# Optimization experiments

Measured on AMD Instinct MI355X. Metric: run time of the kernel, lower is better.

Reference implementation:

```python
import jax, jax.numpy as jnp
import numpy as np
from jax import lax

HEADS = 8
DIM_HEAD = 64
INNER = HEADS * DIM_HEAD  # 512
DIM = 256
TOP_K = 512  # top_k=-1 -> Lk // heads = 4096 // 8
LN_EPS = 1e-5


def chan_ln(x, g, b):
    # LayerNorm over channel dim (axis=1) of [b,c,D,H,W]
    mu = jnp.mean(x, axis=1, keepdims=True)
    var = jnp.mean((x - mu) ** 2, axis=1, keepdims=True)
    xn = (x - mu) * lax.rsqrt(var + LN_EPS)
    return xn * g[None, :, None, None, None] + b[None, :, None, None, None]


def l1_cdist(K, Q):
    # K: [B,N,D], Q: [B,M,D] -> [B,N,M]; scan over feature dim to avoid a [B,N,M,D] intermediate
    Kt = jnp.moveaxis(K, -1, 0)  # [D,B,N]
    Qt = jnp.moveaxis(Q, -1, 0)  # [D,B,M]
    acc0 = jnp.zeros((K.shape[0], K.shape[1], Q.shape[1]), K.dtype)
    def step(acc, kq):
        kd, qd = kq
        return acc + jnp.abs(kd[:, :, None] - qd[:, None, :]), None
    acc, _ = lax.scan(step, acc0, (Kt, Qt))
    return acc


def l2norm_ax(t, axis):
    n = jnp.sqrt(jnp.sum(t * t, axis=axis, keepdims=True))
    return t / jnp.maximum(n, 1e-12)


def setup_inputs() -> dict:
    key = jax.random.key(0)
    ks = jax.random.split(key, 12)
    b, Dq, Hq, Wq = 2, 16, 32, 32
    Dc, Hc, Wc = 16, 16, 16
    Lk = Dc * Hc * Wc  # 4096
    return {
        "query_source": jax.random.normal(ks[0], (b, DIM, Dq, Hq, Wq), jnp.float32),
        "context": jax.random.normal(ks[1], (b, DIM, Dc, Hc, Wc), jnp.float32),
        "rand_idx": jax.random.randint(ks[2], (b * HEADS, TOP_K), 0, 4096),
        "g_ctx": jnp.ones((DIM,), jnp.float32),
        "b_ctx": jnp.zeros((DIM,), jnp.float32),
        "g_qs": jnp.ones((DIM,), jnp.float32),
        "b_qs": jnp.zeros((DIM,), jnp.float32),
        "w_kv": jax.random.normal(ks[3], (2 * INNER, DIM), jnp.float32) * 0.02,
        "w_q": jax.random.normal(ks[4], (INNER, DIM), jnp.float32) * 0.02,
        "w_out": jax.random.normal(ks[5], (DIM, INNER), jnp.float32) * 0.02,
        "g_out": jnp.ones((DIM,), jnp.float32),
        "b_out": jnp.zeros((DIM,), jnp.float32),
        "gamma": jnp.full((1,), 0.5, jnp.float32),
    }


def reference(query_source, context, rand_idx, g_ctx, b_ctx, g_qs, b_qs,
              w_kv, w_q, w_out, g_out, b_out, gamma):
    b, c, Dq, Hq, Wq = query_source.shape
    Lq = Dq * Hq * Wq
    Lk = context.shape[2] * context.shape[3] * context.shape[4]

    ctx = chan_ln(context, g_ctx, b_ctx)
    qsn = chan_ln(query_source, g_qs, b_qs)

    # 1x1x1 convs == channel matmuls
    kv = jnp.einsum('oc,bcdhw->bodhw', w_kv, ctx)
    k, v = jnp.split(kv, 2, axis=1)
    q = jnp.einsum('oc,bcdhw->bodhw', w_q, qsn)

    def fold(t):  # [b, inner, ...] -> [b, heads, dim_head, L]
        return t.reshape(t.shape[0], HEADS, DIM_HEAD, -1)
    q, k, v = fold(q), fold(k), fold(v)
    # l2norm over dim_head channels (torch dim=1 after (b h) fold)
    q = l2norm_ax(q, 2)
    k = l2norm_ax(k, 2)
    # -> [b, heads, L, dim_head]
    q = jnp.swapaxes(q, 2, 3)
    k = jnp.swapaxes(k, 2, 3)
    v = jnp.swapaxes(v, 2, 3)

    BH = b * HEADS
    qf = q.reshape(BH, Lq, DIM_HEAD)
    kf = k.reshape(BH, Lk, DIM_HEAD)
    vf = v.reshape(BH, Lk, DIM_HEAD)

    # random-query-anchored token pruning
    Q_small = jnp.take_along_axis(qf, rand_idx[:, :, None], axis=1)  # [BH, TOP_K, dh]
    dist = l1_cdist(kf, Q_small)                                     # [BH, Lk, TOP_K]
    min_d = jnp.min(dist, axis=2)                                    # [BH, Lk]
    _, idx = lax.top_k(-min_d, TOP_K)                                # smallest distances
    ks_sel = jnp.take_along_axis(kf, idx[:, :, None], axis=1)        # [BH, TOP_K, dh]
    vs_sel = jnp.take_along_axis(vf, idx[:, :, None], axis=1)

    ks4 = ks_sel.reshape(b, HEADS, TOP_K, DIM_HEAD)
    vs4 = vs_sel.reshape(b, HEADS, TOP_K, DIM_HEAD)

    # SDPA with scale=1.0, no dropout (eval)
    scores = jnp.einsum('bhqd,bhkd->bhqk', q, ks4)
    attn = jax.nn.softmax(scores, axis=-1)
    out = jnp.einsum('bhqk,bhkd->bhqd', attn, vs4)  # [b,H,Lq,dh]

    out = out.reshape(b, HEADS, Dq, Hq, Wq, DIM_HEAD)
    out = jnp.transpose(out, (0, 1, 5, 2, 3, 4)).reshape(b, INNER, Dq, Hq, Wq)
    out = jnp.einsum('oc,bcdhw->bodhw', w_out, out)
    out = chan_ln(out, g_out, b_out)
    return gamma[0] * out + query_source
```

## Files before the change

kernel.cpp:

```cpp
#include <hip/hip_runtime.h>
#include <hip/hip_bf16.h>
#include <math.h>

#define DIMC  256
#define HEADS 8
#define DH    64
#define INNER 512
#define TOPK  512
#define LQ    16384
#define LKE   4096
#define NB    2
#define NBH   16

typedef __attribute__((ext_vector_type(8))) short bf16x8;
typedef __attribute__((ext_vector_type(4))) float f32x4;
typedef __attribute__((ext_vector_type(16))) unsigned u32x16;

__device__ __forceinline__ unsigned short f2bf(float f) {
    unsigned u = __float_as_uint(f);
    u += 0x7FFFu + ((u >> 16) & 1u);
    return (unsigned short)(u >> 16);
}
__device__ __forceinline__ float bf2f(unsigned short b) {
    return __uint_as_float(((unsigned)b) << 16);
}
__device__ __forceinline__ f32x4 mfma16(bf16x8 a, bf16x8 b, f32x4 c) {
    return __builtin_amdgcn_mfma_f32_16x16x32_bf16(a, b, c, 0, 0, 0);
}
__device__ __forceinline__ unsigned f2q16(float v) {
    return (unsigned)((int)rintf(v * 32000.0f) + 32768) & 0xFFFFu;
}

__global__ void stats_kernel(const float* __restrict__ x, float* __restrict__ mu,
                             float* __restrict__ rs, int L, int total) {
    int idx = blockIdx.x * 256 + threadIdx.x;
    if (idx >= total) return;
    int b = idx / L, l = idx - b * L;
    const float* p = x + (size_t)b * DIMC * L + l;
    float s = 0.f, sq = 0.f;
    for (int c = 0; c < DIMC; c++) {
        float v = p[(size_t)c * L];
        s += v; sq += v * v;
    }
    float m = s * (1.0f / DIMC);
    float var = fmaxf(sq * (1.0f / DIMC) - m * m, 0.f);
    mu[idx] = m;
    rs[idx] = rsqrtf(var + 1e-5f);
}

template<bool WRITELO>
__global__ __launch_bounds__(256) void ln_transpose_kernel(
    const float* __restrict__ x, const float* __restrict__ mu, const float* __restrict__ rs,
    const float* __restrict__ g, const float* __restrict__ beta, int L,
    unsigned short* __restrict__ xhi, unsigned short* __restrict__ xlo) {
    int lt = blockIdx.x, ct = blockIdx.y, b = blockIdx.z;
    int l0 = lt * 64, c0 = ct * 64;
    int t = threadIdx.x;
    __shared__ float T[64][65];
#pragma unroll
    for (int r = 0; r < 16; r++) {
        int f = r * 256 + t;
        int l = f & 63, c = f >> 6;
        int loc = b * L + l0 + l;
        float v = x[((size_t)b * DIMC + c0 + c) * L + l0 + l];
        T[c][l] = (v - mu[loc]) * rs[loc] * g[c0 + c] + beta[c0 + c];
    }
    __syncthreads();
#pragma unroll
    for (int r = 0; r < 16; r++) {
        int f = r * 256 + t;
        int c = f & 63, l = f >> 6;
        float v = T[c][l];
        unsigned short hi = f2bf(v);
        size_t di = ((size_t)b * L + l0 + l) * DIMC + c0 + c;
        xhi[di] = hi;
        if (WRITELO) xlo[di] = f2bf(v - bf2f(hi));
    }
}

template<int MODE>
__global__ __launch_bounds__(256) void gemm_mfma_kernel(
    const float* __restrict__ wmat,
    const unsigned short* __restrict__ xhi, const unsigned short* __restrict__ xlo,
    void* __restrict__ dst0, void* __restrict__ dst1, void* __restrict__ dst2) {
    constexpr int K = (MODE == 2) ? 512 : 256;
    constexpr int N = (MODE == 0) ? LKE : LQ;
    constexpr bool MAYSPLIT = (MODE == 0);
    int n0 = blockIdx.x * 128;
    int by = blockIdx.y;
    int bb = blockIdx.z;
    int t = threadIdx.x, w = t >> 6, lane = t & 63;
    int wm = w >> 1, wn = w & 1;
    int lanelo = lane & 15, lanehi = lane >> 4;

    __shared__ __align__(16) char Wh[16384];
    __shared__ __align__(16) char Xh[16384];
    __shared__ __align__(16) char Wl[MAYSPLIT ? 16384 : 16];
    __shared__ __align__(16) char Xl[MAYSPLIT ? 16384 : 16];

    bool split = MAYSPLIT && (by < 4);

    const float* wsrc = wmat + (size_t)by * 128 * K;
    const unsigned short* xsh = xhi + ((size_t)bb * N + n0) * K;
    const unsigned short* xsl = xlo + ((size_t)bb * N + n0) * K;

    f32x4 acc[4][4];
#pragma unroll
    for (int mi = 0; mi < 4; mi++)
#pragma unroll
        for (int ni = 0; ni < 4; ni++) acc[mi][ni] = (f32x4){0.f, 0.f, 0.f, 0.f};

    for (int k0 = 0; k0 < K; k0 += 64) {
        if (k0) __syncthreads();
#pragma unroll
        for (int gg = 0; gg < 4; gg++) {
            int e = gg * 2048 + t * 8;
            int row = e >> 6, kc = e & 63;
            const float* wp = wsrc + (size_t)row * K + k0 + kc;
            bf16x8 hi, lo;
#pragma unroll
            for (int i = 0; i < 8; i++) {
                float v = wp[i];
                unsigned short h = f2bf(v);
                hi[i] = (short)h;
                if (MAYSPLIT) lo[i] = (short)f2bf(v - bf2f(h));
            }
            int off = (row * 128 + kc * 2) ^ ((row & 7) << 4);
            *(bf16x8*)(Wh + off) = hi;
            *(bf16x8*)(Xh + off) = *(const bf16x8*)(xsh + (size_t)row * K + k0 + kc);
            if (split) {
                *(bf16x8*)(Wl + off) = lo;
                *(bf16x8*)(Xl + off) = *(const bf16x8*)(xsl + (size_t)row * K + k0 + kc);
            }
        }
        __syncthreads();
#pragma unroll
        for (int kk = 0; kk < 2; kk++) {
            bf16x8 ah[4], bh_[4];
#pragma unroll
            for (int mi = 0; mi < 4; mi++) {
                int row = wm * 64 + mi * 16 + lanelo;
                int off = (row * 128 + kk * 64 + lanehi * 16) ^ ((row & 7) << 4);
                ah[mi] = *(const bf16x8*)(Wh + off);
            }
#pragma unroll
            for (int ni = 0; ni < 4; ni++) {
                int row = wn * 64 + ni * 16 + lanelo;
                int off = (row * 128 + kk * 64 + lanehi * 16) ^ ((row & 7) << 4);
                bh_[ni] = *(const bf16x8*)(Xh + off);
            }
#pragma unroll
            for (int mi = 0; mi < 4; mi++)
#pragma unroll
                for (int ni = 0; ni < 4; ni++)
                    acc[mi][ni] = mfma16(ah[mi], bh_[ni], acc[mi][ni]);
            if (split) {
                bf16x8 al[4], bl_[4];
#pragma unroll
                for (int mi = 0; mi < 4; mi++) {
                    int row = wm * 64 + mi * 16 + lanelo;
                    int off = (row * 128 + kk * 64 + lanehi * 16) ^ ((row & 7) << 4);
                    al[mi] = *(const bf16x8*)(Wl + off);
                }
#pragma unroll
                for (int ni = 0; ni < 4; ni++) {
                    int row = wn * 64 + ni * 16 + lanelo;
                    int off = (row * 128 + kk * 64 + lanehi * 16) ^ ((row & 7) << 4);
                    bl_[ni] = *(const bf16x8*)(Xl + off);
                }
#pragma unroll
                for (int mi = 0; mi < 4; mi++)
#pragma unroll
                    for (int ni = 0; ni < 4; ni++) {
                        acc[mi][ni] = mfma16(ah[mi], bl_[ni], acc[mi][ni]);
                        acc[mi][ni] = mfma16(al[mi], bh_[ni], acc[mi][ni]);
                    }
            }
        }
    }

    bool donorm = (MODE == 1) || (MODE == 0 && by < 4);
    float inv[4];
    if (donorm) {
#pragma unroll
        for (int ni = 0; ni < 4; ni++) {
            float s = 0.f;
#pragma unroll
            for (int mi = 0; mi < 4; mi++)
#pragma unroll
                for (int rg = 0; rg < 4; rg++) s += acc[mi][ni][rg] * acc[mi][ni][rg];
            s += __shfl_xor(s, 16);
            s += __shfl_xor(s, 32);
            inv[ni] = 1.0f / fmaxf(sqrtf(s), 1e-12f);
        }
    }
#pragma unroll
    for (int mi = 0; mi < 4; mi++) {
        int rowg = by * 128 + wm * 64 + mi * 16 + lanehi * 4;
#pragma unroll
        for (int ni = 0; ni < 4; ni++) {
            int l = n0 + wn * 64 + ni * 16 + lanelo;
            if (MODE == 0) {
                bool isk = rowg < 512;
                float sc = isk ? inv[ni] : 1.0f;
                int h = (rowg >> 6) & 7, d0 = rowg & 63;
                float4 v = make_float4(acc[mi][ni][0] * sc, acc[mi][ni][1] * sc,
                                       acc[mi][ni][2] * sc, acc[mi][ni][3] * sc);
                float* dp = isk ? (float*)dst0 : (float*)dst1;
                size_t base = ((size_t)(bb * HEADS + h) * LKE + l) * 64 + d0;
                *(float4*)&dp[base] = v;
                if (isk) {
                    uint2 pk;
                    pk.x = f2q16(v.x) | (f2q16(v.y) << 16);
                    pk.y = f2q16(v.z) | (f2q16(v.w) << 16);
                    *(uint2*)&((unsigned*)dst2)[(((size_t)(bb * HEADS + h) * LKE + l) * 64 + d0) / 2] = pk;
                }
            } else if (MODE == 1) {
                int h = rowg >> 6, d0 = rowg & 63;
                ushort4 u;
                u.x = f2bf(acc[mi][ni][0] * inv[ni]);
                u.y = f2bf(acc[mi][ni][1] * inv[ni]);
                u.z = f2bf(acc[mi][ni][2] * inv[ni]);
                u.w = f2bf(acc[mi][ni][3] * inv[ni]);
                unsigned short* qp = (unsigned short*)dst0;
                *(ushort4*)&qp[((size_t)(bb * HEADS + h) * LQ + l) * 64 + d0] = u;
            } else {
                float4 v = make_float4(acc[mi][ni][0], acc[mi][ni][1],
                                       acc[mi][ni][2], acc[mi][ni][3]);
                float* pp = (float*)dst0;
                *(float4*)&pp[((size_t)bb * LQ + l) * 256 + rowg] = v;
            }
        }
    }
}

__global__ __launch_bounds__(256) void qsample_kernel(
    const float* __restrict__ x, const float* __restrict__ mu, const float* __restrict__ rs,
    const float* __restrict__ g, const float* __restrict__ beta,
    const float* __restrict__ w, const int* __restrict__ ridx,
    unsigned* __restrict__ Qint) {
    int lt = blockIdx.x, bh = blockIdx.y;
    int b = bh >> 3, h = bh & 7;
    int t = threadIdx.x, tx = t & 15, ty = t >> 4;
    __shared__ float Ws[64][33];
    __shared__ float Xs[32][65];
    __shared__ float Cs[64][65];
    __shared__ float nf[64];
    __shared__ int lidx[64];
    if (t < 64) lidx[t] = ridx[bh * TOPK + lt * 64 + t];
    __syncthreads();
    float acc[4][4];
#pragma unroll
    for (int a = 0; a < 4; a++)
#pragma unroll
        for (int c2 = 0; c2 < 4; c2++) acc[a][c2] = 0.f;
    for (int kc = 0; kc < DIMC; kc += 32) {
#pragma unroll
        for (int r = 0; r < 8; r++) {
            int f = r * 256 + t;
            int oi = f >> 5, kj = f & 31;
            Ws[oi][kj] = w[(size_t)(h * 64 + oi) * DIMC + kc + kj];
        }
#pragma unroll
        for (int r = 0; r < 8; r++) {
            int f = r * 256 + t;
            int kj = f >> 6, lj = f & 63;
            int l = lidx[lj];
            int loc = b * LQ + l;
            float v = x[(size_t)b * DIMC * LQ + (size_t)(kc + kj) * LQ + l];
            Xs[kj][lj] = (v - mu[loc]) * rs[loc] * g[kc + kj] + beta[kc + kj];
        }
        __syncthreads();
#pragma unroll
        for (int kj = 0; kj < 32; kj++) {
            float wr[4], xr[4];
#pragma unroll
            for (int a = 0; a < 4; a++) wr[a] = Ws[ty * 4 + a][kj];
#pragma unroll
            for (int c2 = 0; c2 < 4; c2++) xr[c2] = Xs[kj][tx * 4 + c2];
#pragma unroll
            for (int a = 0; a < 4; a++)
#pragma unroll
                for (int c2 = 0; c2 < 4; c2++) acc[a][c2] += wr[a] * xr[c2];
        }
        __syncthreads();
    }
#pragma unroll
    for (int a = 0; a < 4; a++)
#pragma unroll
        for (int c2 = 0; c2 < 4; c2++) Cs[ty * 4 + a][tx * 4 + c2] = acc[a][c2];
    __syncthreads();
    if (t < 64) {
        float sq = 0.f;
        for (int o = 0; o < 64; o++) { float v = Cs[o][t]; sq += v * v; }
        nf[t] = 1.0f / fmaxf(sqrtf(sq), 1e-12f);
    }
    __syncthreads();
#pragma unroll
    for (int r = 0; r < 8; r++) {
        int f = r * 256 + t;
        int dp = f & 31, lj = f >> 5;
        float v0 = Cs[dp * 2][lj] * nf[lj];
        float v1 = Cs[dp * 2 + 1][lj] * nf[lj];
        Qint[((size_t)bh * TOPK + (size_t)lt * 64 + lj) * 32 + dp] =
            f2q16(v0) | (f2q16(v1) << 16);
    }
}

__global__ __launch_bounds__(256) __attribute__((amdgpu_waves_per_eu(4, 4)))
void cdist_sad_kernel(
    const unsigned* __restrict__ kint,
    const unsigned* __restrict__ Qint,
    unsigned* __restrict__ min_d4) {
    int bh = blockIdx.y;
    int key = blockIdx.x * 256 + threadIdx.x;
    int qz = blockIdx.z;
    const unsigned* kp = kint + ((size_t)bh * LKE + key) * 32;
    unsigned k[32];
#pragma unroll
    for (int d8 = 0; d8 < 8; d8++) {
        uint4 v = *(const uint4*)(kp + d8 * 4);
        k[d8 * 4 + 0] = v.x; k[d8 * 4 + 1] = v.y;
        k[d8 * 4 + 2] = v.z; k[d8 * 4 + 3] = v.w;
    }
#pragma unroll
    for (int d = 0; d < 32; d++) asm volatile("" : "+v"(k[d]));

    unsigned long long qaddr = (unsigned long long)(const void*)
        (Qint + ((size_t)bh * TOPK + (size_t)qz * (TOPK / 4)) * 32);
    u32x16 qa0, qa1, qb0, qb1;
    asm volatile(
        "s_load_dwordx16 %0, %2, 0x00\n\t"
        "s_load_dwordx16 %1, %2, 0x40"
        : "=s"(qa0), "=s"(qa1) : "s"(qaddr));
    unsigned best = 0xFFFFFFFFu;

#define S1(ACC, KK, QQ) asm("v_sad_u16 %0, %1, %2, %0" : "+v"(ACC) : "v"(KK), "s"(QQ));
#define S16(QV, KB) \
    S1(a0, k[KB + 0], QV[0])  S1(a1, k[KB + 1], QV[1]) \
    S1(a2, k[KB + 2], QV[2])  S1(a3, k[KB + 3], QV[3]) \
    S1(a0, k[KB + 4], QV[4])  S1(a1, k[KB + 5], QV[5]) \
    S1(a2, k[KB + 6], QV[6])  S1(a3, k[KB + 7], QV[7]) \
    S1(a0, k[KB + 8], QV[8])  S1(a1, k[KB + 9], QV[9]) \
    S1(a2, k[KB + 10], QV[10]) S1(a3, k[KB + 11], QV[11]) \
    S1(a0, k[KB + 12], QV[12]) S1(a1, k[KB + 13], QV[13]) \
    S1(a2, k[KB + 14], QV[14]) S1(a3, k[KB + 15], QV[15])

    for (int qi = 0; qi < TOPK / 4; qi += 2) {
        asm volatile(
            "s_load_dwordx16 %0, %2, 0x80\n\t"
            "s_load_dwordx16 %1, %2, 0xc0"
            : "=s"(qb0), "=s"(qb1) : "s"(qaddr));
        asm volatile("s_waitcnt lgkmcnt(2)" : "+s"(qa0), "+s"(qa1));
        {
            unsigned a0 = 0, a1 = 0, a2 = 0, a3 = 0;
            S16(qa0, 0) S16(qa1, 16)
            best = min(best, (a0 + a1) + (a2 + a3));
        }
        qaddr += 256;
        asm volatile(
            "s_load_dwordx16 %0, %2, 0x00\n\t"
            "s_load_dwordx16 %1, %2, 0x40"
            : "=s"(qa0), "=s"(qa1) : "s"(qaddr));
        asm volatile("s_waitcnt lgkmcnt(2)" : "+s"(qb0), "+s"(qb1));
        {
            unsigned a0 = 0, a1 = 0, a2 = 0, a3 = 0;
            S16(qb0, 0) S16(qb1, 16)
            best = min(best, (a0 + a1) + (a2 + a3));
        }
    }
#undef S16
#undef S1
    min_d4[((size_t)qz * NBH + bh) * LKE + key] = best;
}

__global__ void select_topk_kernel(const unsigned* __restrict__ min_d4, int* __restrict__ isel) {
    int bh = blockIdx.x;
    int t = threadIdx.x;
    __shared__ unsigned su[LKE];
    __shared__ int hist[256];
    __shared__ int sb[2];
    for (int i = t; i < LKE; i += 256) {
        unsigned a = min(min_d4[(size_t)bh * LKE + i],
                         min_d4[(size_t)(NBH + bh) * LKE + i]);
        unsigned b = min(min_d4[(size_t)(2 * NBH + bh) * LKE + i],
                         min_d4[(size_t)(3 * NBH + bh) * LKE + i]);
        su[i] = min(a, b);
    }
    unsigned prefix = 0, mask = 0;
    int need = TOPK;
    for (int shift = 24; shift >= 0; shift -= 8) {
        hist[t] = 0;
        __syncthreads();
        for (int i = t; i < LKE; i += 256) {
            unsigned u = su[i];
            if ((u & mask) == prefix) atomicAdd(&hist[(u >> shift) & 255], 1);
        }
        __syncthreads();
        if (t == 0) {
            int c = 0, bsel = 0;
            for (; bsel < 255; bsel++) {
                if (c + hist[bsel] >= need) break;
                c += hist[bsel];
            }
            sb[0] = bsel; sb[1] = need - c;
        }
        __syncthreads();
        prefix |= ((unsigned)sb[0]) << shift;
        mask |= (255u << shift);
        need = sb[1];
        __syncthreads();
    }
    if (t < 64) {
        int pos = 0, eqseen = 0;
        unsigned long long lanem1 = (t == 0) ? 0ull : ((1ull << t) - 1ull);
        for (int i0 = 0; i0 < LKE; i0 += 64) {
            unsigned u = su[i0 + t];
            bool lt = (u < prefix);
            bool eq = (u == prefix);
            unsigned long long be = __ballot(eq);
            int eqbefore = __popcll(be & lanem1);
            bool take = lt || (eq && (eqseen + eqbefore) < need);
            unsigned long long bt = __ballot(take);
            if (take) isel[bh * TOPK + pos + __popcll(bt & lanem1)] = i0 + t;
            pos += __popcll(bt);
            eqseen += __popcll(be);
        }
    }
}

__global__ void gather_k_kernel(const float* __restrict__ kf, const int* __restrict__ isel,
                                unsigned short* __restrict__ kselh) {
    int idx = blockIdx.x * 256 + threadIdx.x;
    int d = idx & 63;
    int ti = (idx >> 6) & (TOPK - 1);
    int bh = idx >> 15;
    int row = isel[bh * TOPK + ti];
    kselh[idx] = f2bf(kf[((size_t)bh * LKE + row) * 64 + d]);
}

__global__ __launch_bounds__(256) void gather_vT_kernel(
    const float* __restrict__ vf, const int* __restrict__ isel,
    unsigned short* __restrict__ vTh) {
    int bh = blockIdx.y, kc = blockIdx.x * 64;
    int t = threadIdx.x;
    __shared__ float T[64][65];
#pragma unroll
    for (int r = 0; r < 4; r++) {
        int c = r * 256 + t;
        int row = c >> 4, c4 = c & 15;
        int krow = isel[bh * TOPK + kc + row];
        float4 v = *(const float4*)(vf + ((size_t)bh * LKE + krow) * 64 + c4 * 4);
        T[row][c4 * 4 + 0] = v.x; T[row][c4 * 4 + 1] = v.y;
        T[row][c4 * 4 + 2] = v.z; T[row][c4 * 4 + 3] = v.w;
    }
    __syncthreads();
#pragma unroll
    for (int r = 0; r < 16; r++) {
        int f = r * 256 + t;
        int d = f >> 6, key = f & 63;
        vTh[(size_t)bh * 64 * TOPK + (size_t)d * TOPK + kc + key] = f2bf(T[key][d]);
    }
}

__global__ __launch_bounds__(256) void attn_mfma_kernel(
    const unsigned short* __restrict__ qh,
    const unsigned short* __restrict__ kselh,
    const unsigned short* __restrict__ vTh,
    unsigned short* __restrict__ afT) {
    int bh = blockIdx.y, rt = blockIdx.x;
    int bq = bh >> 3, h = bh & 7;
    int t = threadIdx.x, w = t >> 6, lane = t & 63;
    __shared__ unsigned short Qs[64 * 64];
    __shared__ unsigned short Ks[2][64 * 64];
    __shared__ unsigned short Vts[2][64 * 64];
    __shared__ unsigned short Ps[4 * 16 * 64];

    const unsigned short* qb = qh + ((size_t)bh * LQ + (size_t)rt * 64) * 64;
    const unsigned short* kb = kselh + (size_t)bh * TOPK * 64;
    const unsigned short* vb = vTh + (size_t)bh * 64 * TOPK;

    int row0s = t >> 3, c80 = t & 7;
    int row1s = 32 + (t >> 3), c81 = t & 7;
    int offs0 = (row0s * 128 + c80 * 16) ^ ((row0s & 7) << 4);
    int offs1 = (row1s * 128 + c81 * 16) ^ ((row1s & 7) << 4);

    {
        bf16x8 v0 = *(const bf16x8*)(qb + row0s * 64 + c80 * 8);
        bf16x8 v1 = *(const bf16x8*)(qb + row1s * 64 + c81 * 8);
        *(bf16x8*)((char*)Qs + offs0) = v0;
        *(bf16x8*)((char*)Qs + offs1) = v1;
    }
    {
        bf16x8 k0 = *(const bf16x8*)(kb + row0s * 64 + c80 * 8);
        bf16x8 k1 = *(const bf16x8*)(kb + row1s * 64 + c81 * 8);
        bf16x8 v0 = *(const bf16x8*)(vb + row0s * TOPK + c80 * 8);
        bf16x8 v1 = *(const bf16x8*)(vb + row1s * TOPK + c81 * 8);
        *(bf16x8*)((char*)Ks[0] + offs0) = k0;
        *(bf16x8*)((char*)Ks[0] + offs1) = k1;
        *(bf16x8*)((char*)Vts[0] + offs0) = v0;
        *(bf16x8*)((char*)Vts[0] + offs1) = v1;
    }
    __syncthreads();

    bf16x8 qfrag[2];
#pragma unroll
    for (int kk = 0; kk < 2; kk++) {
        int row = w * 16 + (lane & 15);
        qfrag[kk] = *(const bf16x8*)((char*)Qs +
            ((row * 128 + kk * 64 + (lane >> 4) * 16) ^ ((row & 7) << 4)));
    }

    f32x4 o[4];
#pragma unroll
    for (int m = 0; m < 4; m++) o[m] = (f32x4){0.f, 0.f, 0.f, 0.f};
    float part[4] = {0.f, 0.f, 0.f, 0.f};
    unsigned short* pw = Ps + w * 16 * 64;
    int cur = 0;

    for (int ch = 0; ch < 8; ch++) {
        bf16x8 knx0, knx1, vnx0, vnx1;
        if (ch < 7) {
            int kc0 = (ch + 1) * 64;
            knx0 = *(const bf16x8*)(kb + (kc0 + row0s) * 64 + c80 * 8);
            knx1 = *(const bf16x8*)(kb + (kc0 + row1s) * 64 + c81 * 8);
            vnx0 = *(const bf16x8*)(vb + row0s * TOPK + kc0 + c80 * 8);
            vnx1 = *(const bf16x8*)(vb + row1s * TOPK + kc0 + c81 * 8);
        }
        f32x4 s[4];
#pragma unroll
        for (int n = 0; n < 4; n++) {
            s[n] = (f32x4){0.f, 0.f, 0.f, 0.f};
#pragma unroll
            for (int kk = 0; kk < 2; kk++) {
                int row = n * 16 + (lane & 15);
                bf16x8 kfr = *(const bf16x8*)((char*)Ks[cur] +
                    ((row * 128 + kk * 64 + (lane >> 4) * 16) ^ ((row & 7) << 4)));
                s[n] = mfma16(qfrag[kk], kfr, s[n]);
            }
        }
#pragma unroll
        for (int n = 0; n < 4; n++) {
#pragma unroll
            for (int rg = 0; rg < 4; rg++) {
                float p = __expf(s[n][rg]);
                part[rg] += p;
                int row = (lane >> 4) * 4 + rg, col = n * 16 + (lane & 15);
                *(unsigned short*)((char*)pw +
                    ((row * 128 + col * 2) ^ ((row & 7) << 4))) = f2bf(p);
            }
        }
        bf16x8 pfrag[2];
#pragma unroll
        for (int kk = 0; kk < 2; kk++) {
            int row = lane & 15;
            pfrag[kk] = *(const bf16x8*)((char*)pw +
                ((row * 128 + kk * 64 + (lane >> 4) * 16) ^ ((row & 7) << 4)));
        }
#pragma unroll
        for (int m = 0; m < 4; m++) {
#pragma unroll
            for (int kk = 0; kk < 2; kk++) {
                int row = m * 16 + (lane & 15);
                bf16x8 vfr = *(const bf16x8*)((char*)Vts[cur] +
                    ((row * 128 + kk * 64 + (lane >> 4) * 16) ^ ((row & 7) << 4)));
                o[m] = mfma16(pfrag[kk], vfr, o[m]);
            }
        }
        if (ch < 7) {
            *(bf16x8*)((char*)Ks[cur ^ 1] + offs0) = knx0;
            *(bf16x8*)((char*)Ks[cur ^ 1] + offs1) = knx1;
            *(bf16x8*)((char*)Vts[cur ^ 1] + offs0) = vnx0;
            *(bf16x8*)((char*)Vts[cur ^ 1] + offs1) = vnx1;
        }
        __syncthreads();
        cur ^= 1;
    }
    float lsum[4];
#pragma unroll
    for (int rg = 0; rg < 4; rg++) {
        float v = part[rg];
        v += __shfl_xor(v, 1); v += __shfl_xor(v, 2);
        v += __shfl_xor(v, 4); v += __shfl_xor(v, 8);
        lsum[rg] = v;
    }
    int row0 = w * 16 + (lane >> 4) * 4;
#pragma unroll
    for (int rg = 0; rg < 4; rg++) {
        float invs = 1.0f / lsum[rg];
        int l = rt * 64 + row0 + rg;
        size_t base = ((size_t)bq * LQ + l) * 512 + h * 64 + (lane & 15);
#pragma unroll
        for (int m = 0; m < 4; m++)
            afT[base + m * 16] = f2bf(o[m][rg] * invs);
    }
}

__global__ void stats_loc_kernel(const float* __restrict__ pre, float* __restrict__ mu,
                                 float* __restrict__ rs) {
    int t = threadIdx.x;
    int grp = t >> 4, ln = t & 15;
    int loc = blockIdx.x * 16 + grp;
    const float4* p = (const float4*)(pre + (size_t)loc * 256);
    float s = 0.f, sq = 0.f;
#pragma unroll
    for (int i = 0; i < 4; i++) {
        float4 v = p[ln + i * 16];
        s += v.x + v.y + v.z + v.w;
        sq += v.x * v.x + v.y * v.y + v.z * v.z + v.w * v.w;
    }
#pragma unroll
    for (int d = 1; d < 16; d <<= 1) {
        s += __shfl_xor(s, d);
        sq += __shfl_xor(sq, d);
    }
    if (ln == 0) {
        float m = s * (1.0f / 256.0f);
        float var = fmaxf(sq * (1.0f / 256.0f) - m * m, 0.f);
        mu[loc] = m;
        rs[loc] = rsqrtf(var + 1e-5f);
    }
}

__global__ __launch_bounds__(256) void final_kernel(
    const float* __restrict__ pre, const float* __restrict__ mu,
    const float* __restrict__ rs, const float* __restrict__ g,
    const float* __restrict__ beta, const float* __restrict__ gamma,
    const float* __restrict__ qs_in, float* __restrict__ out) {
    int lt = blockIdx.x, ot = blockIdx.y, b = blockIdx.z;
    int l0 = lt * 64, o0 = ot * 64;
    int t = threadIdx.x;
    __shared__ float T[64][65];
    float gm = gamma[0];
#pragma unroll
    for (int r = 0; r < 16; r++) {
        int f = r * 256 + t;
        int o = f & 63, l = f >> 6;
        int loc = b * LQ + l0 + l;
        float v = pre[(size_t)loc * 256 + o0 + o];
        T[o][l] = ((v - mu[loc]) * rs[loc] * g[o0 + o] + beta[o0 + o]) * gm;
    }
    __syncthreads();
#pragma unroll
    for (int r = 0; r < 16; r++) {
        int f = r * 256 + t;
        int l = f & 63, o = f >> 6;
        size_t oi = ((size_t)(b * DIMC + o0 + o)) * LQ + l0 + l;
        out[oi] = T[o][l] + qs_in[oi];
    }
}

extern "C" void kernel_launch(void* const* d_in, const int* in_sizes, int n_in,
                              void* d_out, int out_size, void* d_ws, size_t ws_size,
                              hipStream_t stream) {
    const float* qs_in = (const float*)d_in[0];
    const float* ctx   = (const float*)d_in[1];
    const int*   ridx  = (const int*)d_in[2];
    const float* g_ctx = (const float*)d_in[3];
    const float* b_ctx = (const float*)d_in[4];
    const float* g_qs  = (const float*)d_in[5];
    const float* b_qs  = (const float*)d_in[6];
    const float* w_kv  = (const float*)d_in[7];
    const float* w_q   = (const float*)d_in[8];
    const float* w_out = (const float*)d_in[9];
    const float* g_out = (const float*)d_in[10];
    const float* b_out = (const float*)d_in[11];
    const float* gamma = (const float*)d_in[12];
    float* out = (float*)d_out;

    char* ws = (char*)d_ws;
    size_t off = 0;
    auto alloc = [&](size_t bytes) { char* p = ws + off; off += (bytes + 255) & ~(size_t)255; return p; };

    float*          kf    = (float*)alloc((size_t)NBH * LKE * 64 * 4);
    float*          vf    = (float*)alloc((size_t)NBH * LKE * 64 * 4);
    unsigned*       kint  = (unsigned*)alloc((size_t)NBH * LKE * 32 * 4);
    unsigned short* qh    = (unsigned short*)alloc((size_t)NBH * LQ * 64 * 2);
    char*           uni   = alloc((size_t)NB * LQ * INNER * 2);
    unsigned short* ctxT_hi = (unsigned short*)(uni);
    unsigned short* ctxT_lo = (unsigned short*)(uni + (size_t)NB * LKE * DIMC * 2);
    unsigned short* qsT_hi  = (unsigned short*)(uni + (size_t)2 * NB * LKE * DIMC * 2);
    unsigned short* afT     = (unsigned short*)(uni);

    unsigned*       Qint  = (unsigned*)alloc((size_t)NBH * TOPK * 32 * 4);
    unsigned short* kselh = (unsigned short*)alloc((size_t)NBH * TOPK * 64 * 2);
    unsigned short* vTh   = (unsigned short*)alloc((size_t)NBH * 64 * TOPK * 2);
    float*          pre   = (float*)alloc((size_t)NB * LQ * DIMC * 4);
    unsigned*       min_d4= (unsigned*)alloc((size_t)4 * NBH * LKE * 4);
    float*          mu_c  = (float*)alloc(NB * LKE * 4);
    float*          rs_c  = (float*)alloc(NB * LKE * 4);
    float*          mu_q  = (float*)alloc(NB * LQ * 4);
    float*          rs_q  = (float*)alloc(NB * LQ * 4);
    float*          mu_o  = (float*)alloc(NB * LQ * 4);
    float*          rs_o  = (float*)alloc(NB * LQ * 4);
    int*            isel  = (int*)alloc(NBH * TOPK * 4);

    stats_kernel<<<(NB * LKE + 255) / 256, 256, 0, stream>>>(ctx, mu_c, rs_c, LKE, NB * LKE);
    stats_kernel<<<(NB * LQ + 255) / 256, 256, 0, stream>>>(qs_in, mu_q, rs_q, LQ, NB * LQ);
    ln_transpose_kernel<true><<<dim3(LKE / 64, DIMC / 64, NB), 256, 0, stream>>>(
        ctx, mu_c, rs_c, g_ctx, b_ctx, LKE, ctxT_hi, ctxT_lo);
    ln_transpose_kernel<false><<<dim3(LQ / 64, DIMC / 64, NB), 256, 0, stream>>>(
        qs_in, mu_q, rs_q, g_qs, b_qs, LQ, qsT_hi, nullptr);
    gemm_mfma_kernel<0><<<dim3(LKE / 128, 8, NB), 256, 0, stream>>>(
        w_kv, ctxT_hi, ctxT_lo, kf, vf, kint);
    gemm_mfma_kernel<1><<<dim3(LQ / 128, 4, NB), 256, 0, stream>>>(
        w_q, qsT_hi, qsT_hi, qh, nullptr, nullptr);
    qsample_kernel<<<dim3(TOPK / 64, NBH), 256, 0, stream>>>(
        qs_in, mu_q, rs_q, g_qs, b_qs, w_q, ridx, Qint);
    cdist_sad_kernel<<<dim3(LKE / 256, NBH, 4), 256, 0, stream>>>(kint, Qint, min_d4);
    select_topk_kernel<<<NBH, 256, 0, stream>>>(min_d4, isel);
    gather_k_kernel<<<(NBH * TOPK * 64) / 256, 256, 0, stream>>>(kf, isel, kselh);
    gather_vT_kernel<<<dim3(TOPK / 64, NBH), 256, 0, stream>>>(vf, isel, vTh);
    attn_mfma_kernel<<<dim3(LQ / 64, NBH), 256, 0, stream>>>(qh, kselh, vTh, afT);
    gemm_mfma_kernel<2><<<dim3(LQ / 128, 2, NB), 256, 0, stream>>>(
        w_out, afT, afT, pre, nullptr, nullptr);
    stats_loc_kernel<<<(NB * LQ) / 16, 256, 0, stream>>>(pre, mu_o, rs_o);
    final_kernel<<<dim3(LQ / 64, DIMC / 64, NB), 256, 0, stream>>>(
        pre, mu_o, rs_o, g_out, b_out, gamma, qs_in, out);
}
```

Baseline: 343.8 us.

## Process 128 query rows per attention block and reuse K/V fragments across halves

The attention kernel now handles 128 query rows per block instead of 64. Each wave holds two 16-row query slices in registers, loaded directly from global memory, so the shared Q tile is gone. K and V fragments are read from LDS once per chunk and used for both slices, which halves LDS traffic and global K/V loads per query row. The cost is more registers per thread and half as many blocks (2048 instead of 4096), which may reduce occupancy.

Result: no change. 341.3 us (-0.7%).

```diff
diff --git a/kernel.cpp b/kernel.cpp
--- a/kernel.cpp
+++ b/kernel.cpp
@@ -471,51 +471,44 @@
     int bh = blockIdx.y, rt = blockIdx.x;
     int bq = bh >> 3, h = bh & 7;
     int t = threadIdx.x, w = t >> 6, lane = t & 63;
-    __shared__ unsigned short Qs[64 * 64];
     __shared__ unsigned short Ks[2][64 * 64];
     __shared__ unsigned short Vts[2][64 * 64];
-    __shared__ unsigned short Ps[4 * 16 * 64];
-
-    const unsigned short* qb = qh + ((size_t)bh * LQ + (size_t)rt * 64) * 64;
+    __shared__ unsigned short Ps[4][2][16 * 64];
+
+    const unsigned short* qb = qh + ((size_t)bh * LQ + (size_t)rt * 128) * 64;
     const unsigned short* kb = kselh + (size_t)bh * TOPK * 64;
     const unsigned short* vb = vTh + (size_t)bh * 64 * TOPK;
+
+    int lanelo = lane & 15, lanehi = lane >> 4;
 
     int row0s = t >> 3, c80 = t & 7;
     int row1s = 32 + (t >> 3), c81 = t & 7;
     int offs0 = (row0s * 128 + c80 * 16) ^ ((row0s & 7) << 4);
     int offs1 = (row1s * 128 + c81 * 16) ^ ((row1s & 7) << 4);
 
+    bf16x8 qfrag[2][2];
+#pragma unroll
+    for (int s = 0; s < 2; s++)
+#pragma unroll
+        for (int kk = 0; kk < 2; kk++) {
+            int row = s * 64 + w * 16 + lanelo;
+            qfrag[s][kk] = *(const bf16x8*)(qb + (size_t)row * 64 + kk * 32 + lanehi * 8);
+        }
+
     {
-        bf16x8 v0 = *(const bf16x8*)(qb + row0s * 64 + c80 * 8);
-        bf16x8 v1 = *(const bf16x8*)(qb + row1s * 64 + c81 * 8);
-        *(bf16x8*)((char*)Qs + offs0) = v0;
-        *(bf16x8*)((char*)Qs + offs1) = v1;
-    }
-    {
-        bf16x8 k0 = *(const bf16x8*)(kb + row0s * 64 + c80 * 8);
-        bf16x8 k1 = *(const bf16x8*)(kb + row1s * 64 + c81 * 8);
-        bf16x8 v0 = *(const bf16x8*)(vb + row0s * TOPK + c80 * 8);
-        bf16x8 v1 = *(const bf16x8*)(vb + row1s * TOPK + c81 * 8);
-        *(bf16x8*)((char*)Ks[0] + offs0) = k0;
-        *(bf16x8*)((char*)Ks[0] + offs1) = k1;
-        *(bf16x8*)((char*)Vts[0] + offs0) = v0;
-        *(bf16x8*)((char*)Vts[0] + offs1) = v1;
+        *(bf16x8*)((char*)Ks[0] + offs0) = *(const bf16x8*)(kb + row0s * 64 + c80 * 8);
+        *(bf16x8*)((char*)Ks[0] + offs1) = *(const bf16x8*)(kb + row1s * 64 + c81 * 8);
+        *(bf16x8*)((char*)Vts[0] + offs0) = *(const bf16x8*)(vb + row0s * TOPK + c80 * 8);
+        *(bf16x8*)((char*)Vts[0] + offs1) = *(const bf16x8*)(vb + row1s * TOPK + c81 * 8);
     }
     __syncthreads();
 
-    bf16x8 qfrag[2];
-#pragma unroll
-    for (int kk = 0; kk < 2; kk++) {
-        int row = w * 16 + (lane & 15);
-        qfrag[kk] = *(const bf16x8*)((char*)Qs +
-            ((row * 128 + kk * 64 + (lane >> 4) * 16) ^ ((row & 7) << 4)));
-    }
-
-    f32x4 o[4];
-#pragma unroll
-    for (int m = 0; m < 4; m++) o[m] = (f32x4){0.f, 0.f, 0.f, 0.f};
-    float part[4] = {0.f, 0.f, 0.f, 0.f};
-    unsigned short* pw = Ps + w * 16 * 64;
+    f32x4 o[2][4];
+#pragma unroll
+    for (int s = 0; s < 2; s++)
+#pragma unroll
+        for (int m = 0; m < 4; m++) o[s][m] = (f32x4){0.f, 0.f, 0.f, 0.f};
+    float part[2][4] = {{0.f, 0.f, 0.f, 0.f}, {0.f, 0.f, 0.f, 0.f}};
     int cur = 0;
 
     for (int ch = 0; ch < 8; ch++) {
@@ -527,45 +520,61 @@
             vnx0 = *(const bf16x8*)(vb + row0s * TOPK + kc0 + c80 * 8);
             vnx1 = *(const bf16x8*)(vb + row1s * TOPK + kc0 + c81 * 8);
         }
-        f32x4 s[4];
-#pragma unroll
-        for (int n = 0; n < 4; n++) {
-            s[n] = (f32x4){0.f, 0.f, 0.f, 0.f};
+        bf16x8 kfr[4][2];
+#pragma unroll
+        for (int n = 0; n < 4; n++)
 #pragma unroll
             for (int kk = 0; kk < 2; kk++) {
-                int row = n * 16 + (lane & 15);
-                bf16x8 kfr = *(const bf16x8*)((char*)Ks[cur] +
-                    ((row * 128 + kk * 64 + (lane >> 4) * 16) ^ ((row & 7) << 4)));
-                s[n] = mfma16(qfrag[kk], kfr, s[n]);
-            }
-        }
-#pragma unroll
-        for (int n = 0; n < 4; n++) {
-#pragma unroll
-            for (int rg = 0; rg < 4; rg++) {
-                float p = __expf(s[n][rg]);
-                part[rg] += p;
-                int row = (lane >> 4) * 4 + rg, col = n * 16 + (lane & 15);
-                *(unsigned short*)((char*)pw +
-                    ((row * 128 + col * 2) ^ ((row & 7) << 4))) = f2bf(p);
-            }
-        }
-        bf16x8 pfrag[2];
-#pragma unroll
-        for (int kk = 0; kk < 2; kk++) {
-            int row = lane & 15;
-            pfrag[kk] = *(const bf16x8*)((char*)pw +
-                ((row * 128 + kk * 64 + (lane >> 4) * 16) ^ ((row & 7) << 4)));
-        }
-#pragma unroll
-        for (int m = 0; m < 4; m++) {
+                int row = n * 16 + lanelo;
+                kfr[n][kk] = *(const bf16x8*)((char*)Ks[cur] +
+                    ((row * 128 + kk * 64 + lanehi * 16) ^ ((row & 7) << 4)));
+            }
+#pragma unroll
+        for (int s = 0; s < 2; s++) {
+            f32x4 sv[4];
+#pragma unroll
+            for (int n = 0; n < 4; n++) {
+                sv[n] = (f32x4){0.f, 0.f, 0.f, 0.f};
+#pragma unroll
+                for (int kk = 0; kk < 2; kk++)
+                    sv[n] = mfma16(qfrag[s][kk], kfr[n][kk], sv[n]);
+            }
+            unsigned short* pw = Ps[w][s];
+#pragma unroll
+            for (int n = 0; n < 4; n++) {
+#pragma unroll
+                for (int rg = 0; rg < 4; rg++) {
+                    float p = __expf(sv[n][rg]);
+                    part[s][rg] += p;
+                    int row = lanehi * 4 + rg, col = n * 16 + lanelo;
+                    *(unsigned short*)((char*)pw +
+                        ((row * 128 + col * 2) ^ ((row & 7) << 4))) = f2bf(p);
+                }
+            }
+        }
+        bf16x8 vfr[4][2];
+#pragma unroll
+        for (int m = 0; m < 4; m++)
 #pragma unroll
             for (int kk = 0; kk < 2; kk++) {
-                int row = m * 16 + (lane & 15);
-                bf16x8 vfr = *(const bf16x8*)((char*)Vts[cur] +
-                    ((row * 128 + kk * 64 + (lane >> 4) * 16) ^ ((row & 7) << 4)));
-                o[m] = mfma16(pfrag[kk], vfr, o[m]);
-            }
+                int row = m * 16 + lanelo;
+                vfr[m][kk] = *(const bf16x8*)((char*)Vts[cur] +
+                    ((row * 128 + kk * 64 + lanehi * 16) ^ ((row & 7) << 4)));
+            }
+#pragma unroll
+        for (int s = 0; s < 2; s++) {
+            bf16x8 pfrag[2];
+#pragma unroll
+            for (int kk = 0; kk < 2; kk++) {
+                int row = lanelo;
+                pfrag[kk] = *(const bf16x8*)((char*)Ps[w][s] +
+                    ((row * 128 + kk * 64 + lanehi * 16) ^ ((row & 7) << 4)));
+            }
+#pragma unroll
+            for (int m = 0; m < 4; m++)
+#pragma unroll
+                for (int kk = 0; kk < 2; kk++)
+                    o[s][m] = mfma16(pfrag[kk], vfr[m][kk], o[s][m]);
         }
         if (ch < 7) {
             *(bf16x8*)((char*)Ks[cur ^ 1] + offs0) = knx0;
@@ -576,23 +585,20 @@
         __syncthreads();
         cur ^= 1;
     }
-    float lsum[4];
-#pragma unroll
-    for (int rg = 0; rg < 4; rg++) {
-        float v = part[rg];
-        v += __shfl_xor(v, 1); v += __shfl_xor(v, 2);
-        v += __shfl_xor(v, 4); v += __shfl_xor(v, 8);
-        lsum[rg] = v;
-    }
-    int row0 = w * 16 + (lane >> 4) * 4;
-#pragma unroll
-    for (int rg = 0; rg < 4; rg++) {
-        float invs = 1.0f / lsum[rg];
-        int l = rt * 64 + row0 + rg;
-        size_t base = ((size_t)bq * LQ + l) * 512 + h * 64 + (lane & 15);
-#pragma unroll
-        for (int m = 0; m < 4; m++)
-            afT[base + m * 16] = f2bf(o[m][rg] * invs);
+#pragma unroll
+    for (int s = 0; s < 2; s++) {
+#pragma unroll
+        for (int rg = 0; rg < 4; rg++) {
+            float v = part[s][rg];
+            v += __shfl_xor(v, 1); v += __shfl_xor(v, 2);
+            v += __shfl_xor(v, 4); v += __shfl_xor(v, 8);
+            float invs = 1.0f / v;
+            int l = rt * 128 + s * 64 + w * 16 + lanehi * 4 + rg;
+            size_t base = ((size_t)bq * LQ + l) * 512 + h * 64 + lanelo;
+#pragma unroll
+            for (int m = 0; m < 4; m++)
+                afT[base + m * 16] = f2bf(o[s][m][rg] * invs);
+        }
     }
 }
 
@@ -711,7 +717,7 @@
     select_topk_kernel<<<NBH, 256, 0, stream>>>(min_d4, isel);
     gather_k_kernel<<<(NBH * TOPK * 64) / 256, 256, 0, stream>>>(kf, isel, kselh);
     gather_vT_kernel<<<dim3(TOPK / 64, NBH), 256, 0, stream>>>(vf, isel, vTh);
-    attn_mfma_kernel<<<dim3(LQ / 64, NBH), 256, 0, stream>>>(qh, kselh, vTh, afT);
+    attn_mfma_kernel<<<dim3(LQ / 128, NBH), 256, 0, stream>>>(qh, kselh, vTh, afT);
     gemm_mfma_kernel<2><<<dim3(LQ / 128, 2, NB), 256, 0, stream>>>(
         w_out, afT, afT, pre, nullptr, nullptr);
     stats_loc_kernel<<<(NB * LQ) / 16, 256, 0, stream>>>(pre, mu_o, rs_o);
```
